# Kernel tuning notes

Hardware: AMD Instinct MI355X
Metric: run time of the kernel (lower is better)

## Reference

```python
import jax, jax.numpy as jnp
import numpy as np

B, S, H, N = 16, 256, 128, 64  # batch, max_seq_length, hidden_size, num_neurons


def setup_inputs() -> dict:
    key = jax.random.key(0)
    k1, k2 = jax.random.split(key)
    inputs = jax.random.normal(k1, (B, S, H), dtype=jnp.float32)
    threshes = jax.random.uniform(k2, (N,), dtype=jnp.float32)  # torch.rand(num_neurons)
    acc0 = jnp.zeros((B, N), dtype=jnp.float32)  # initial accumulations state
    return {"inputs": inputs, "threshes": threshes, "acc0": acc0}


def reference(inputs, threshes, acc0):
    # The torch double loop over (i, j) is a single sequential chain of T = S*H
    # steps through `accumulations`; express it as one lax.scan.
    b, s, h = inputs.shape
    xs = inputs.reshape(b, s * h).T  # [T, B] in (i, j) order

    def step(acc, x):  # acc: [B, N], x: [B]
        acc = acc + x[:, None]                 # broadcast scalar input to all neurons
        spike = acc > threshes                 # [B, N] bool
        out = jnp.where(spike, acc, jnp.float32(0))  # spike * accumulations
        return acc - out, (out, spike)         # reset fired neurons

    _, (outs, spikes) = jax.lax.scan(step, acc0, xs)
    # outs/spikes: [T, B, N] -> [S, H, B, N] -> [B, S, N, H] (matches torch stack order)
    outs = outs.reshape(s, h, b, -1).transpose(2, 0, 3, 1)
    spikes = spikes.reshape(s, h, b, -1).transpose(2, 0, 3, 1)
    return outs, spikes
```

## Files before the change

### kernel.cpp

```cpp
#include <hip/hip_runtime.h>


namespace {
constexpr int kB = 16;
constexpr int kS = 256;
constexpr int kH = 128;
constexpr int kN = 64;
constexpr int kT = kS * kH;
constexpr long kPerB = (long)kS * kN * kH;
constexpr size_t kWsS = (size_t)kB * kS * kN * sizeof(float);
constexpr size_t kWsM = (size_t)kB * kS * sizeof(unsigned long long);
}

typedef float v4f __attribute__((ext_vector_type(4)));

__device__ __forceinline__ int opaque_vgpr_zero() {
  int z;
  asm volatile("v_mov_b32 %0, 0" : "=v"(z));
  return z;
}

__device__ __forceinline__ void load16(v4f (&buf)[16], const v4f* __restrict__ p) {
#pragma unroll
  for (int i = 0; i < 16; ++i) buf[i] = p[i];
}

__device__ __forceinline__ void consume64(const v4f (&buf)[16], float& s,
                                          bool& prev, float th) {
#pragma unroll
  for (int k = 0; k < 64; ++k) {
    const float xt = buf[k >> 2][k & 3];
    const float u = s + xt;
    s = prev ? xt : u;
    prev = s > th;
  }
}

__global__ __launch_bounds__(64, 1) void lif_pass1_kernel(
    const float* __restrict__ x, const float* __restrict__ thresh,
    const float* __restrict__ acc0, float* __restrict__ ckpt_s,
    unsigned long long* __restrict__ ckpt_m) {
  const int b = blockIdx.x;
  const int lane = threadIdx.x;
  const float th = thresh[lane];

  const v4f* __restrict__ xb4 =
      (const v4f*)(x + (long)b * kT) + opaque_vgpr_zero();

  float s = acc0[b * kN + lane];
  bool prev = false;

  v4f A[16], Bv[16], C[16], D[16];
  load16(A, xb4 + 0 * 16);
  load16(Bv, xb4 + 1 * 16);
  load16(C, xb4 + 2 * 16);
  load16(D, xb4 + 3 * 16);

  float* __restrict__ cs = ckpt_s + (long)b * kS * kN + lane;
  unsigned long long* __restrict__ cm = ckpt_m + (long)b * kS;

  for (int g = 0; g < 128; ++g) {
    const int c0 = 4 * g;
    const v4f* pA = xb4 + 16 * (c0 + 4 < 512 ? c0 + 4 : 511);
    const v4f* pB = xb4 + 16 * (c0 + 5 < 512 ? c0 + 5 : 511);
    const v4f* pC = xb4 + 16 * (c0 + 6 < 512 ? c0 + 6 : 511);
    const v4f* pD = xb4 + 16 * (c0 + 7 < 512 ? c0 + 7 : 511);

    cs[(long)(2 * g) * kN] = s;
    {
      const unsigned long long m = __ballot(prev);
      if (lane == 0) cm[2 * g] = m;
    }
    consume64(A, s, prev, th);
    load16(A, pA);
    consume64(Bv, s, prev, th);
    load16(Bv, pB);

    cs[(long)(2 * g + 1) * kN] = s;
    {
      const unsigned long long m = __ballot(prev);
      if (lane == 0) cm[2 * g + 1] = m;
    }
    consume64(C, s, prev, th);
    load16(C, pC);
    consume64(D, s, prev, th);
    load16(D, pD);
  }
}

__global__ __launch_bounds__(64) void lif_pass2_kernel(
    const float* __restrict__ x, const float* __restrict__ thresh,
    const float* __restrict__ ckpt_s,
    const unsigned long long* __restrict__ ckpt_m, float* __restrict__ out) {
  const int wid = blockIdx.x;
  const int b = wid >> 8;
  const int srow = wid & 255;
  const int lane = threadIdx.x;

  __shared__ float ov[kH][kN + 1];

  const v4f* __restrict__ xr4 =
      (const v4f*)(x + (long)b * kT + srow * kH) + opaque_vgpr_zero();

  v4f xb[32];
#pragma unroll
  for (int i = 0; i < 32; ++i) xb[i] = xr4[i];

  const float th = thresh[lane];
  float s = ckpt_s[((long)b * kS + srow) * kN + lane];
  bool prev = (ckpt_m[b * kS + srow] >> lane) & 1ULL;

#pragma unroll
  for (int h = 0; h < kH; ++h) {
    const float xt = xb[h >> 2][h & 3];
    const float u = s + xt;
    s = prev ? xt : u;
    prev = s > th;
    ov[h][lane] = prev ? s : 0.0f;
  }
  __syncthreads();

  float* __restrict__ obase = out + (long)b * kPerB + (long)srow * (kN * kH);
  float* __restrict__ sbase = obase + (long)kB * kPerB;
  const int h0 = (lane & 31) * 4;
  const int nhalf = lane >> 5;
#pragma unroll
  for (int i = 0; i < 32; ++i) {
    const int n = i * 2 + nhalf;
    v4f o, sp;
#pragma unroll
    for (int j = 0; j < 4; ++j) {
      const float v = ov[h0 + j][n];
      o[j] = v;
      sp[j] = v > 0.0f ? 1.0f : 0.0f;
    }
    __builtin_nontemporal_store(o, (v4f*)(obase + n * kH + h0));
    __builtin_nontemporal_store(sp, (v4f*)(sbase + n * kH + h0));
  }
}

__global__ __launch_bounds__(128) void lif_fused_kernel(
    const float* __restrict__ x, const float* __restrict__ thresh,
    const float* __restrict__ acc0, float* __restrict__ out) {
  const int bid = blockIdx.x;
  const int b = bid >> 2;
  const int ng = bid & 3;
  const int tid = threadIdx.x;
  const int wave = tid >> 6;
  const int lane = tid & 63;
  __shared__ float buf[2][kH][64];
  const float* __restrict__ xb = x + (long)b * kT;
  float* __restrict__ outs_g = out + (long)b * kPerB + (long)(ng * 16) * kH;
  float* __restrict__ spks_g = outs_g + (long)kB * kPerB;
  if (wave == 0) {
    const int n = lane & 15;
    const float th = thresh[ng * 16 + n];
    float s = acc0[b * kN + ng * 16 + n];
    bool prev = false;
    for (int r = 0; r < kS + 1; ++r) {
      if (r < kS) {
        float* __restrict__ bk = &buf[r & 1][0][lane];
        const float* __restrict__ xr = xb + r * kH;
#pragma unroll
        for (int k = 0; k < kH; ++k) {
          const float xt = xr[k];
          const float u = s + xt;
          s = prev ? xt : u;
          prev = s > th;
          bk[k * 64] = s;
        }
      }
      __syncthreads();
    }
  } else {
    const int n = lane >> 2;
    const int hg = lane & 3;
    const float th = thresh[ng * 16 + n];
    for (int r = 0; r < kS + 1; ++r) {
      if (r > 0) {
        const int rr = r - 1;
        const float(*bk)[64] = buf[rr & 1];
        float* __restrict__ orow = outs_g + (long)rr * (kN * kH) + n * kH;
        float* __restrict__ srow = spks_g + (long)rr * (kN * kH) + n * kH;
#pragma unroll
        for (int i = 0; i < 8; ++i) {
          const int hh = hg * 4 + i * 16;
          v4f ovv, sv;
#pragma unroll
          for (int j = 0; j < 4; ++j) {
            const float v = bk[hh + j][n];
            const bool sp = v > th;
            ovv[j] = sp ? v : 0.0f;
            sv[j] = sp ? 1.0f : 0.0f;
          }
          *(v4f*)(orow + hh) = ovv;
          *(v4f*)(srow + hh) = sv;
        }
      }
      __syncthreads();
    }
  }
}

extern "C" void kernel_launch(void* const* d_in, const int* in_sizes, int n_in,
                              void* d_out, int out_size, void* d_ws, size_t ws_size,
                              hipStream_t stream) {
  const float* inputs = (const float*)d_in[0];
  const float* threshes = (const float*)d_in[1];
  const float* acc0 = (const float*)d_in[2];
  float* out = (float*)d_out;

  if (ws_size >= kWsS + kWsM) {
    float* ckpt_s = (float*)d_ws;
    unsigned long long* ckpt_m = (unsigned long long*)((char*)d_ws + kWsS);
    lif_pass1_kernel<<<kB, kN, 0, stream>>>(inputs, threshes, acc0, ckpt_s,
                                            ckpt_m);
    lif_pass2_kernel<<<kB * kS, kN, 0, stream>>>(inputs, threshes, ckpt_s,
                                                 ckpt_m, out);
  } else {
    lif_fused_kernel<<<kB * 4, 128, 0, stream>>>(inputs, threshes, acc0, out);
  }
}
```

Measured before the change: 600.3 us.

## Stage pass1 inputs through LDS in chunks and halve pass2 shared buffer

```diff
diff --git a/kernel.cpp b/kernel.cpp
--- a/kernel.cpp
+++ b/kernel.cpp
@@ -8,6 +8,7 @@
 constexpr int kN = 64;
 constexpr int kT = kS * kH;
 constexpr long kPerB = (long)kS * kN * kH;
+constexpr int kQ = 8192;
 constexpr size_t kWsS = (size_t)kB * kS * kN * sizeof(float);
 constexpr size_t kWsM = (size_t)kB * kS * sizeof(unsigned long long);
 }
@@ -18,22 +19,6 @@
   int z;
   asm volatile("v_mov_b32 %0, 0" : "=v"(z));
   return z;
-}
-
-__device__ __forceinline__ void load16(v4f (&buf)[16], const v4f* __restrict__ p) {
-#pragma unroll
-  for (int i = 0; i < 16; ++i) buf[i] = p[i];
-}
-
-__device__ __forceinline__ void consume64(const v4f (&buf)[16], float& s,
-                                          bool& prev, float th) {
-#pragma unroll
-  for (int k = 0; k < 64; ++k) {
-    const float xt = buf[k >> 2][k & 3];
-    const float u = s + xt;
-    s = prev ? xt : u;
-    prev = s > th;
-  }
 }
 
 __global__ __launch_bounds__(64, 1) void lif_pass1_kernel(
@@ -44,51 +29,51 @@
   const int lane = threadIdx.x;
   const float th = thresh[lane];
 
-  const v4f* __restrict__ xb4 =
+  __shared__ v4f xs[kQ / 4];
+
+  const v4f* __restrict__ xg =
       (const v4f*)(x + (long)b * kT) + opaque_vgpr_zero();
 
   float s = acc0[b * kN + lane];
   bool prev = false;
 
-  v4f A[16], Bv[16], C[16], D[16];
-  load16(A, xb4 + 0 * 16);
-  load16(Bv, xb4 + 1 * 16);
-  load16(C, xb4 + 2 * 16);
-  load16(D, xb4 + 3 * 16);
-
   float* __restrict__ cs = ckpt_s + (long)b * kS * kN + lane;
   unsigned long long* __restrict__ cm = ckpt_m + (long)b * kS;
 
-  for (int g = 0; g < 128; ++g) {
-    const int c0 = 4 * g;
-    const v4f* pA = xb4 + 16 * (c0 + 4 < 512 ? c0 + 4 : 511);
-    const v4f* pB = xb4 + 16 * (c0 + 5 < 512 ? c0 + 5 : 511);
-    const v4f* pC = xb4 + 16 * (c0 + 6 < 512 ? c0 + 6 : 511);
-    const v4f* pD = xb4 + 16 * (c0 + 7 < 512 ? c0 + 7 : 511);
-
-    cs[(long)(2 * g) * kN] = s;
+  for (int q = 0; q < 4; ++q) {
     {
-      const unsigned long long m = __ballot(prev);
-      if (lane == 0) cm[2 * g] = m;
-    }
-    consume64(A, s, prev, th);
-    load16(A, pA);
-    consume64(Bv, s, prev, th);
-    load16(Bv, pB);
-
-    cs[(long)(2 * g + 1) * kN] = s;
-    {
-      const unsigned long long m = __ballot(prev);
-      if (lane == 0) cm[2 * g + 1] = m;
-    }
-    consume64(C, s, prev, th);
-    load16(C, pC);
-    consume64(D, s, prev, th);
-    load16(D, pD);
-  }
-}
-
-__global__ __launch_bounds__(64) void lif_pass2_kernel(
+      const v4f* __restrict__ src = xg + (long)q * (kQ / 4) + lane;
+      v4f tmp[32];
+#pragma unroll
+      for (int i = 0; i < 32; ++i) tmp[i] = src[i * 64];
+#pragma unroll
+      for (int i = 0; i < 32; ++i) xs[i * 64 + lane] = tmp[i];
+    }
+
+    for (int jrow = 0; jrow < 64; ++jrow) {
+      const int r = q * 64 + jrow;
+      cs[(long)r * kN] = s;
+      {
+        const unsigned long long m = __ballot(prev);
+        if (lane == 0) cm[r] = m;
+      }
+      const v4f* __restrict__ xr = &xs[jrow * 32];
+#pragma unroll
+      for (int k = 0; k < 32; ++k) {
+        const v4f xv = xr[k];
+#pragma unroll
+        for (int j = 0; j < 4; ++j) {
+          const float xt = xv[j];
+          const float u = s + xt;
+          s = prev ? xt : u;
+          prev = s > th;
+        }
+      }
+    }
+  }
+}
+
+__global__ __launch_bounds__(64, 2) void lif_pass2_kernel(
     const float* __restrict__ x, const float* __restrict__ thresh,
     const float* __restrict__ ckpt_s,
     const unsigned long long* __restrict__ ckpt_m, float* __restrict__ out) {
@@ -97,7 +82,7 @@
   const int srow = wid & 255;
   const int lane = threadIdx.x;
 
-  __shared__ float ov[kH][kN + 1];
+  __shared__ float ov[kH / 2][kN + 1];
 
   const v4f* __restrict__ xr4 =
       (const v4f*)(x + (long)b * kT + srow * kH) + opaque_vgpr_zero();
@@ -110,32 +95,36 @@
   float s = ckpt_s[((long)b * kS + srow) * kN + lane];
   bool prev = (ckpt_m[b * kS + srow] >> lane) & 1ULL;
 
-#pragma unroll
-  for (int h = 0; h < kH; ++h) {
-    const float xt = xb[h >> 2][h & 3];
-    const float u = s + xt;
-    s = prev ? xt : u;
-    prev = s > th;
-    ov[h][lane] = prev ? s : 0.0f;
-  }
-  __syncthreads();
-
   float* __restrict__ obase = out + (long)b * kPerB + (long)srow * (kN * kH);
   float* __restrict__ sbase = obase + (long)kB * kPerB;
-  const int h0 = (lane & 31) * 4;
-  const int nhalf = lane >> 5;
-#pragma unroll
-  for (int i = 0; i < 32; ++i) {
-    const int n = i * 2 + nhalf;
-    v4f o, sp;
-#pragma unroll
-    for (int j = 0; j < 4; ++j) {
-      const float v = ov[h0 + j][n];
-      o[j] = v;
-      sp[j] = v > 0.0f ? 1.0f : 0.0f;
-    }
-    __builtin_nontemporal_store(o, (v4f*)(obase + n * kH + h0));
-    __builtin_nontemporal_store(sp, (v4f*)(sbase + n * kH + h0));
+
+#pragma unroll
+  for (int half = 0; half < 2; ++half) {
+#pragma unroll
+    for (int hh = 0; hh < kH / 2; ++hh) {
+      const int h = half * (kH / 2) + hh;
+      const float xt = xb[h >> 2][h & 3];
+      const float u = s + xt;
+      s = prev ? xt : u;
+      prev = s > th;
+      ov[hh][lane] = prev ? s : 0.0f;
+    }
+    const int q = lane & 15;
+    const int nsub = lane >> 4;
+    const int h0 = half * (kH / 2) + q * 4;
+#pragma unroll
+    for (int i = 0; i < 16; ++i) {
+      const int n = i * 4 + nsub;
+      v4f o, sp;
+#pragma unroll
+      for (int j = 0; j < 4; ++j) {
+        const float v = ov[q * 4 + j][n];
+        o[j] = v;
+        sp[j] = v > 0.0f ? 1.0f : 0.0f;
+      }
+      *(v4f*)(obase + (long)n * kH + h0) = o;
+      *(v4f*)(sbase + (long)n * kH + h0) = sp;
+    }
   }
 }
 
```

Result: slower. 637.9 us (+6.3%).
